# Optimization experiments

Hardware: AMD Instinct MI355X
Metric: run time of the kernel (lower is better)

Reference implementation:

```python
import jax, jax.numpy as jnp
import numpy as np

N_NODES = 100000
N_EDGES = 1600000
DIMS = [64, 64, 64, 32]  # [n_feat] + hid


def setup_inputs() -> dict:
    key = jax.random.key(0)
    ks = jax.random.split(key, 2 + 2 * (len(DIMS) - 1))
    x = jax.random.normal(ks[0], (N_NODES, DIMS[0]), dtype=jnp.float32)
    edge_index = jax.random.randint(ks[1], (2, N_EDGES), 0, N_NODES, dtype=jnp.int64)
    inp = {"x": x, "edge_index": edge_index}
    for i in range(len(DIMS) - 1):
        fan_in, fan_out = DIMS[i], DIMS[i + 1]
        scale = 1.0 / np.sqrt(fan_in)
        inp[f"W{i+1}"] = jax.random.normal(ks[2 + 2 * i], (fan_in, fan_out), dtype=jnp.float32) * scale
        inp[f"b{i+1}"] = jax.random.normal(ks[3 + 2 * i], (fan_out,), dtype=jnp.float32) * scale
    return inp


def _gcn_conv(x, W, b, src, dst, dis):
    # h = X W ; out[i] = sum_{j->i} norm_ij * h[j] + dis[i]^2 * h[i] + b
    h = x @ W
    norm = dis[src] * dis[dst]                      # [E]
    agg = jax.ops.segment_sum(h[src] * norm[:, None], dst, num_segments=x.shape[0])
    agg = agg + h * (dis * dis)[:, None]            # self-loop contribution
    return agg + b


def reference(x, edge_index, W1, b1, W2, b2, W3, b3):
    src, dst = edge_index[0], edge_index[1]
    n = x.shape[0]
    # degree with self-loops (edge weight 1), symmetric normalization
    deg = jax.ops.segment_sum(jnp.ones(src.shape[0], x.dtype), dst, num_segments=n) + 1.0
    dis = jax.lax.rsqrt(deg)
    h = jax.nn.relu(_gcn_conv(x, W1, b1, src, dst, dis))   # dropout is identity in eval
    h = jax.nn.relu(_gcn_conv(h, W2, b2, src, dst, dis))
    return _gcn_conv(h, W3, b3, src, dst, dis)
```

## Files before the change

### kernel.cpp

```cpp
#include <hip/hip_runtime.h>


typedef __attribute__((ext_vector_type(8))) _Float16 half8;
typedef __attribute__((ext_vector_type(4))) _Float16 half4;

static inline int cdiv(int a, int b) { return (a + b - 1) / b; }

#define ACHUNK 2048
#define BSHIFT 7
#define BMASK 127
#define MAXNBK 1024
#define SCAN_CHUNK 1024
#define BCAP 4096

__global__ __launch_bounds__(256)
void k_bucket_hist(const int* __restrict__ dst, int* __restrict__ counts_t,
                   int NBK, int NBA, int E) {
    __shared__ int cnt[MAXNBK];
    int t = threadIdx.x, b = blockIdx.x;
    for (int i = t; i < NBK; i += 256) cnt[i] = 0;
    __syncthreads();
    int e0 = b * ACHUNK;
#pragma unroll 8
    for (int j = 0; j < ACHUNK / 256; ++j) {
        int e = e0 + j * 256 + t;
        if (e < E) atomicAdd(&cnt[dst[e] >> BSHIFT], 1);
    }
    __syncthreads();
    for (int i = t; i < NBK; i += 256) counts_t[i * NBA + b] = cnt[i];
}

__global__ __launch_bounds__(256)
void k_scan_partial(const int* __restrict__ a, int* __restrict__ bsum, int n) {
    __shared__ int red[256];
    int t = threadIdx.x, b = blockIdx.x;
    int base = b * SCAN_CHUNK + t * 4;
    int s = 0;
#pragma unroll
    for (int j = 0; j < 4; ++j) { int i = base + j; if (i < n) s += a[i]; }
    red[t] = s;
    __syncthreads();
    for (int off = 128; off > 0; off >>= 1) {
        if (t < off) red[t] += red[t + off];
        __syncthreads();
    }
    if (t == 0) bsum[b] = red[0];
}

__global__ __launch_bounds__(256)
void k_scan_final(const int* __restrict__ a, const int* __restrict__ bsum,
                  int* __restrict__ out, int nb, int n) {
    __shared__ int sh[256];
    __shared__ int bb;
    int t = threadIdx.x, bk = blockIdx.x;
    int bv[4];
    int bt = 0;
#pragma unroll
    for (int j = 0; j < 4; ++j) {
        int i = 4 * t + j;
        bv[j] = (i < nb) ? bsum[i] : 0;
        bt += bv[j];
    }
    sh[t] = bt;
    __syncthreads();
    for (int off = 1; off < 256; off <<= 1) {
        int u = (t >= off) ? sh[t - off] : 0;
        __syncthreads();
        sh[t] += u;
        __syncthreads();
    }
    int bexcl = sh[t] - bt;
    if (bk == 0) {
        if (t == 0) bb = 0;
    } else {
        int q = bk - 1;
        if (t == (q >> 2)) {
            int s = bexcl;
#pragma unroll
            for (int j = 0; j < 4; ++j)
                if (j <= (q & 3)) s += bv[j];
            bb = s;
        }
    }
    __syncthreads();
    int bbase = bb;
    __syncthreads();
    int base = bk * SCAN_CHUNK + t * 4;
    int v[4];
    int s = 0;
#pragma unroll
    for (int j = 0; j < 4; ++j) {
        int i = base + j;
        v[j] = (i < n) ? a[i] : 0;
        s += v[j];
    }
    sh[t] = s;
    __syncthreads();
    for (int off = 1; off < 256; off <<= 1) {
        int u = (t >= off) ? sh[t - off] : 0;
        __syncthreads();
        sh[t] += u;
        __syncthreads();
    }
    int run = sh[t] - s + bbase;
#pragma unroll
    for (int j = 0; j < 4; ++j) {
        int i = base + j;
        if (i < n) { out[i] = run; run += v[j]; }
    }
}

__global__ __launch_bounds__(256)
void k_bucket_scatter(const int* __restrict__ src, const int* __restrict__ dst,
                      const int* __restrict__ offsets, unsigned* __restrict__ bucketed,
                      int NBK, int NBA, int E) {
    __shared__ int curs[MAXNBK];
    int t = threadIdx.x, b = blockIdx.x;
    for (int i = t; i < NBK; i += 256) curs[i] = offsets[i * NBA + b];
    __syncthreads();
    int e0 = b * ACHUNK;
#pragma unroll 8
    for (int j = 0; j < ACHUNK / 256; ++j) {
        int e = e0 + j * 256 + t;
        if (e < E) {
            int d = dst[e];
            int pos = atomicAdd(&curs[d >> BSHIFT], 1);
            bucketed[pos] = (unsigned)src[e] | ((unsigned)(d & BMASK) << 24);
        }
    }
}

__global__ __launch_bounds__(256)
void k_bucket_build(const unsigned* __restrict__ bucketed,
                    const int* __restrict__ offsets,
                    int* __restrict__ csr_src, int* __restrict__ row_start,
                    float* __restrict__ dis, int NBK, int NBA, int N, int E) {
    __shared__ int cnt[128];
    __shared__ int sc[128];
    __shared__ int srt[BCAP];
    int t = threadIdx.x, k = blockIdx.x;
    int base = offsets[k * NBA];
    int end = (k + 1 < NBK) ? offsets[(k + 1) * NBA] : E;
    if (t < 128) cnt[t] = 0;
    __syncthreads();
    for (int i = base + t; i < end; i += 256)
        atomicAdd(&cnt[bucketed[i] >> 24], 1);
    __syncthreads();
    int c = 0;
    if (t < 128) { c = cnt[t]; sc[t] = c; }
    __syncthreads();
    for (int off = 1; off < 128; off <<= 1) {
        int u = (t >= off && t < 128) ? sc[t - off] : 0;
        __syncthreads();
        if (t < 128) sc[t] += u;
        __syncthreads();
    }
    if (t < 128) {
        int excl = sc[t] - c;
        int node = (k << BSHIFT) + t;
        if (node < N) {
            row_start[node] = base + excl;
            dis[node] = rsqrtf(1.0f + (float)c);
        }
        cnt[t] = excl;
    }
    if (k == 0 && t == 0) row_start[N] = E;
    __syncthreads();
    int m = end - base;
    if (m <= BCAP) {
        for (int i = base + t; i < end; i += 256) {
            unsigned w = bucketed[i];
            int r = atomicAdd(&cnt[w >> 24], 1);
            srt[r] = (int)(w & 0xFFFFFFu);
        }
        __syncthreads();
        for (int idx = t; idx < m; idx += 256)
            csr_src[base + idx] = srt[idx];
    } else {
        for (int i = base + t; i < end; i += 256) {
            unsigned w = bucketed[i];
            int pos = base + atomicAdd(&cnt[w >> 24], 1);
            csr_src[pos] = (int)(w & 0xFFFFFFu);
        }
    }
}

template <int K, int M>
__global__ void k_gemm_f(const float* __restrict__ X, const float* __restrict__ W,
                         const float* __restrict__ dis, _Float16* __restrict__ H, int n) {
    constexpr int TPR = M / 8;
    constexpr int ROWS = 256 / TPR;
    constexpr int KP = K + 1;
    __shared__ float Ws[K * M];
    __shared__ float Xs[ROWS * KP];
    int tid = threadIdx.x;
    for (int idx = tid; idx < K * M / 4; idx += 256)
        ((float4*)Ws)[idx] = ((const float4*)W)[idx];
    int row0 = blockIdx.x * ROWS;
    for (int idx = tid; idx < ROWS * (K / 4); idx += 256) {
        int r = idx / (K / 4), kq = idx % (K / 4);
        int row = row0 + r;
        float4 vv = (row < n) ? ((const float4*)X)[(size_t)row * (K / 4) + kq]
                              : make_float4(0.f, 0.f, 0.f, 0.f);
        Xs[r * KP + kq * 4 + 0] = vv.x;
        Xs[r * KP + kq * 4 + 1] = vv.y;
        Xs[r * KP + kq * 4 + 2] = vv.z;
        Xs[r * KP + kq * 4 + 3] = vv.w;
    }
    __syncthreads();
    int r = tid / TPR, c0 = (tid % TPR) * 8;
    int row = row0 + r;
    if (row >= n) return;
    float4 a0 = make_float4(0.f, 0.f, 0.f, 0.f);
    float4 a1 = make_float4(0.f, 0.f, 0.f, 0.f);
#pragma unroll
    for (int k = 0; k < K; ++k) {
        float xv = Xs[r * KP + k];
        float4 w0 = ((const float4*)Ws)[(k * M + c0) / 4];
        float4 w1 = ((const float4*)Ws)[(k * M + c0) / 4 + 1];
        a0.x = fmaf(xv, w0.x, a0.x);
        a0.y = fmaf(xv, w0.y, a0.y);
        a0.z = fmaf(xv, w0.z, a0.z);
        a0.w = fmaf(xv, w0.w, a0.w);
        a1.x = fmaf(xv, w1.x, a1.x);
        a1.y = fmaf(xv, w1.y, a1.y);
        a1.z = fmaf(xv, w1.z, a1.z);
        a1.w = fmaf(xv, w1.w, a1.w);
    }
    float dn = dis[row];
    half8 hv;
    hv[0] = (_Float16)(a0.x * dn);
    hv[1] = (_Float16)(a0.y * dn);
    hv[2] = (_Float16)(a0.z * dn);
    hv[3] = (_Float16)(a0.w * dn);
    hv[4] = (_Float16)(a1.x * dn);
    hv[5] = (_Float16)(a1.y * dn);
    hv[6] = (_Float16)(a1.z * dn);
    hv[7] = (_Float16)(a1.w * dn);
    ((half8*)H)[(size_t)row * (M / 8) + c0 / 8] = hv;
}

template <int MOUT>
__global__ __launch_bounds__(256, 8)
void k_fused_agg_gemm(const _Float16* __restrict__ h, const float* __restrict__ dis,
                      const int* __restrict__ row_start, const int* __restrict__ csr_src,
                      const float* __restrict__ bagg, const float* __restrict__ W,
                      _Float16* __restrict__ H, int n) {
    constexpr int K = 64, KP = K + 1;
    __shared__ __align__(16) _Float16 Ws[K * MOUT];
    __shared__ float Xs[32 * KP];
    int tid = threadIdx.x;
    for (int idx = tid; idx < K * MOUT / 4; idx += 256) {
        float4 wv = ((const float4*)W)[idx];
        half4 h4;
        h4[0] = (_Float16)wv.x;
        h4[1] = (_Float16)wv.y;
        h4[2] = (_Float16)wv.z;
        h4[3] = (_Float16)wv.w;
        ((half4*)Ws)[idx] = h4;
    }

    int wave = tid >> 6, lane = tid & 63;
    int sub = lane >> 3, fl = lane & 7;
    int node0 = blockIdx.x * 32;
    int node = node0 + wave * 8 + sub;
    if (node < n) {
        const half8* h8 = (const half8*)h;
        float acc[8];
#pragma unroll
        for (int j = 0; j < 8; ++j) acc[j] = 0.f;
        int e = row_start[node], e1 = row_start[node + 1];
        for (; e + 7 < e1; e += 8) {
            int s0 = csr_src[e], s1 = csr_src[e + 1];
            int s2 = csr_src[e + 2], s3 = csr_src[e + 3];
            int s4 = csr_src[e + 4], s5 = csr_src[e + 5];
            int s6 = csr_src[e + 6], s7 = csr_src[e + 7];
            half8 v0 = h8[(size_t)s0 * 8 + fl];
            half8 v1 = h8[(size_t)s1 * 8 + fl];
            half8 v2 = h8[(size_t)s2 * 8 + fl];
            half8 v3 = h8[(size_t)s3 * 8 + fl];
            half8 v4 = h8[(size_t)s4 * 8 + fl];
            half8 v5 = h8[(size_t)s5 * 8 + fl];
            half8 v6 = h8[(size_t)s6 * 8 + fl];
            half8 v7 = h8[(size_t)s7 * 8 + fl];
#pragma unroll
            for (int j = 0; j < 8; ++j)
                acc[j] += (((float)v0[j] + (float)v1[j]) + ((float)v2[j] + (float)v3[j])) +
                          (((float)v4[j] + (float)v5[j]) + ((float)v6[j] + (float)v7[j]));
        }
        for (; e + 3 < e1; e += 4) {
            int s0 = csr_src[e], s1 = csr_src[e + 1];
            int s2 = csr_src[e + 2], s3 = csr_src[e + 3];
            half8 v0 = h8[(size_t)s0 * 8 + fl];
            half8 v1 = h8[(size_t)s1 * 8 + fl];
            half8 v2 = h8[(size_t)s2 * 8 + fl];
            half8 v3 = h8[(size_t)s3 * 8 + fl];
#pragma unroll
            for (int j = 0; j < 8; ++j)
                acc[j] += ((float)v0[j] + (float)v1[j]) + ((float)v2[j] + (float)v3[j]);
        }
        for (; e < e1; ++e) {
            int s0 = csr_src[e];
            half8 v0 = h8[(size_t)s0 * 8 + fl];
#pragma unroll
            for (int j = 0; j < 8; ++j) acc[j] += (float)v0[j];
        }
        float dn = dis[node];
        half8 hv = h8[(size_t)node * 8 + fl];
        float4 b0 = ((const float4*)bagg)[fl * 2];
        float4 b1 = ((const float4*)bagg)[fl * 2 + 1];
        int rrow = wave * 8 + sub;
        float* xp = &Xs[rrow * KP + fl * 8];
        xp[0] = fmaxf((acc[0] + (float)hv[0]) * dn + b0.x, 0.f);
        xp[1] = fmaxf((acc[1] + (float)hv[1]) * dn + b0.y, 0.f);
        xp[2] = fmaxf((acc[2] + (float)hv[2]) * dn + b0.z, 0.f);
        xp[3] = fmaxf((acc[3] + (float)hv[3]) * dn + b0.w, 0.f);
        xp[4] = fmaxf((acc[4] + (float)hv[4]) * dn + b1.x, 0.f);
        xp[5] = fmaxf((acc[5] + (float)hv[5]) * dn + b1.y, 0.f);
        xp[6] = fmaxf((acc[6] + (float)hv[6]) * dn + b1.z, 0.f);
        xp[7] = fmaxf((acc[7] + (float)hv[7]) * dn + b1.w, 0.f);
    }
    __syncthreads();

    constexpr int TPR = 8;
    constexpr int CPT = MOUT / TPR;
    int r = tid / TPR, c0 = (tid % TPR) * CPT;
    int row = node0 + r;
    if (row >= n) return;
    float4 a0 = make_float4(0.f, 0.f, 0.f, 0.f);
    float4 a1 = make_float4(0.f, 0.f, 0.f, 0.f);
#pragma unroll
    for (int k = 0; k < K; ++k) {
        float xv = Xs[r * KP + k];
        if constexpr (CPT == 8) {
            half8 w = ((const half8*)Ws)[(k * MOUT + c0) / 8];
            a0.x = fmaf(xv, (float)w[0], a0.x);
            a0.y = fmaf(xv, (float)w[1], a0.y);
            a0.z = fmaf(xv, (float)w[2], a0.z);
            a0.w = fmaf(xv, (float)w[3], a0.w);
            a1.x = fmaf(xv, (float)w[4], a1.x);
            a1.y = fmaf(xv, (float)w[5], a1.y);
            a1.z = fmaf(xv, (float)w[6], a1.z);
            a1.w = fmaf(xv, (float)w[7], a1.w);
        } else {
            half4 w = ((const half4*)Ws)[(k * MOUT + c0) / 4];
            a0.x = fmaf(xv, (float)w[0], a0.x);
            a0.y = fmaf(xv, (float)w[1], a0.y);
            a0.z = fmaf(xv, (float)w[2], a0.z);
            a0.w = fmaf(xv, (float)w[3], a0.w);
        }
    }
    float dn = dis[row];
    if constexpr (CPT == 8) {
        half8 hv;
        hv[0] = (_Float16)(a0.x * dn);
        hv[1] = (_Float16)(a0.y * dn);
        hv[2] = (_Float16)(a0.z * dn);
        hv[3] = (_Float16)(a0.w * dn);
        hv[4] = (_Float16)(a1.x * dn);
        hv[5] = (_Float16)(a1.y * dn);
        hv[6] = (_Float16)(a1.z * dn);
        hv[7] = (_Float16)(a1.w * dn);
        ((half8*)H)[(size_t)row * (MOUT / 8) + c0 / 8] = hv;
    } else {
        half4 hv;
        hv[0] = (_Float16)(a0.x * dn);
        hv[1] = (_Float16)(a0.y * dn);
        hv[2] = (_Float16)(a0.z * dn);
        hv[3] = (_Float16)(a0.w * dn);
        ((half4*)H)[(size_t)row * (MOUT / 4) + c0 / 4] = hv;
    }
}

__global__ __launch_bounds__(256, 8)
void k_aggregate32(const _Float16* __restrict__ h, const float* __restrict__ dis,
                   const int* __restrict__ row_start, const int* __restrict__ csr_src,
                   const float* __restrict__ b, float* __restrict__ out, int n) {
    constexpr int LPN = 4, NPW = 16;
    int gtid = blockIdx.x * blockDim.x + threadIdx.x;
    int wave = gtid >> 6;
    int lane = threadIdx.x & 63;
    int sub = lane / LPN, fl = lane % LPN;
    int node = wave * NPW + sub;
    if (node >= n) return;
    const half8* h8 = (const half8*)h;
    float acc[8];
#pragma unroll
    for (int j = 0; j < 8; ++j) acc[j] = 0.f;
    int e = row_start[node], e1 = row_start[node + 1];
    for (; e + 7 < e1; e += 8) {
        int s0 = csr_src[e], s1 = csr_src[e + 1];
        int s2 = csr_src[e + 2], s3 = csr_src[e + 3];
        int s4 = csr_src[e + 4], s5 = csr_src[e + 5];
        int s6 = csr_src[e + 6], s7 = csr_src[e + 7];
        half8 v0 = h8[(size_t)s0 * LPN + fl];
        half8 v1 = h8[(size_t)s1 * LPN + fl];
        half8 v2 = h8[(size_t)s2 * LPN + fl];
        half8 v3 = h8[(size_t)s3 * LPN + fl];
        half8 v4 = h8[(size_t)s4 * LPN + fl];
        half8 v5 = h8[(size_t)s5 * LPN + fl];
        half8 v6 = h8[(size_t)s6 * LPN + fl];
        half8 v7 = h8[(size_t)s7 * LPN + fl];
#pragma unroll
        for (int j = 0; j < 8; ++j)
            acc[j] += (((float)v0[j] + (float)v1[j]) + ((float)v2[j] + (float)v3[j])) +
                      (((float)v4[j] + (float)v5[j]) + ((float)v6[j] + (float)v7[j]));
    }
    for (; e + 3 < e1; e += 4) {
        int s0 = csr_src[e], s1 = csr_src[e + 1];
        int s2 = csr_src[e + 2], s3 = csr_src[e + 3];
        half8 v0 = h8[(size_t)s0 * LPN + fl];
        half8 v1 = h8[(size_t)s1 * LPN + fl];
        half8 v2 = h8[(size_t)s2 * LPN + fl];
        half8 v3 = h8[(size_t)s3 * LPN + fl];
#pragma unroll
        for (int j = 0; j < 8; ++j)
            acc[j] += ((float)v0[j] + (float)v1[j]) + ((float)v2[j] + (float)v3[j]);
    }
    for (; e < e1; ++e) {
        int s0 = csr_src[e];
        half8 v0 = h8[(size_t)s0 * LPN + fl];
#pragma unroll
        for (int j = 0; j < 8; ++j) acc[j] += (float)v0[j];
    }
    float dn = dis[node];
    half8 hv = h8[(size_t)node * LPN + fl];
    float4 b0 = ((const float4*)b)[fl * 2];
    float4 b1 = ((const float4*)b)[fl * 2 + 1];
    float4* op = (float4*)(out + ((size_t)node * LPN + fl) * 8);
    op[0] = make_float4((acc[0] + (float)hv[0]) * dn + b0.x,
                        (acc[1] + (float)hv[1]) * dn + b0.y,
                        (acc[2] + (float)hv[2]) * dn + b0.z,
                        (acc[3] + (float)hv[3]) * dn + b0.w);
    op[1] = make_float4((acc[4] + (float)hv[4]) * dn + b1.x,
                        (acc[5] + (float)hv[5]) * dn + b1.y,
                        (acc[6] + (float)hv[6]) * dn + b1.z,
                        (acc[7] + (float)hv[7]) * dn + b1.w);
}

extern "C" void kernel_launch(void* const* d_in, const int* in_sizes, int n_in,
                              void* d_out, int out_size, void* d_ws, size_t ws_size,
                              hipStream_t stream) {
    const float* x   = (const float*)d_in[0];
    const int*   ei  = (const int*)d_in[1];
    const float* W1  = (const float*)d_in[2];
    const float* b1  = (const float*)d_in[3];
    const float* W2  = (const float*)d_in[4];
    const float* b2  = (const float*)d_in[5];
    const float* W3  = (const float*)d_in[6];
    const float* b3  = (const float*)d_in[7];
    float* out = (float*)d_out;

    const int N = in_sizes[0] / 64;
    const int E = in_sizes[1] / 2;
    const int* src = ei;
    const int* dst = ei + E;

    const int NBK = cdiv(N, 128);
    const int NBA = cdiv(E, ACHUNK);
    const int nmat = NBK * NBA;
    const int nb = cdiv(nmat, SCAN_CHUNK);

    const size_t Np = (size_t)((N + 63) / 64) * 64;
    char* p = (char*)d_ws;
    int*      counts_t = (int*)p;      p += (size_t)nmat * sizeof(int);
    int*      offsets  = (int*)p;      p += (size_t)nmat * sizeof(int);
    int*      bsum     = (int*)p;      p += 1024 * sizeof(int);
    int*      row_start= (int*)p;      p += (Np + 64) * sizeof(int);
    float*    dis      = (float*)p;    p += Np * sizeof(float);
    unsigned* bucketed = (unsigned*)p; p += (size_t)E * sizeof(unsigned);
    int*      csr_src  = (int*)p;      p += (size_t)E * sizeof(int);
    _Float16* bufA     = (_Float16*)p; p += Np * 64 * sizeof(_Float16);
    _Float16* bufB     = (_Float16*)p; p += Np * 64 * sizeof(_Float16);
    (void)ws_size;

    const int B = 256;

    k_bucket_hist<<<NBA, B, 0, stream>>>(dst, counts_t, NBK, NBA, E);
    k_scan_partial<<<nb, B, 0, stream>>>(counts_t, bsum, nmat);
    k_scan_final<<<nb, B, 0, stream>>>(counts_t, bsum, offsets, nb, nmat);
    k_bucket_scatter<<<NBA, B, 0, stream>>>(src, dst, offsets, bucketed, NBK, NBA, E);
    k_bucket_build<<<NBK, B, 0, stream>>>(bucketed, offsets, csr_src, row_start, dis,
                                          NBK, NBA, N, E);

    k_gemm_f<64, 64><<<cdiv(N, 32), B, 0, stream>>>(x, W1, dis, bufA, N);
    k_fused_agg_gemm<64><<<cdiv(N, 32), B, 0, stream>>>(
        bufA, dis, row_start, csr_src, b1, W2, bufB, N);
    k_fused_agg_gemm<32><<<cdiv(N, 32), B, 0, stream>>>(
        bufB, dis, row_start, csr_src, b2, W3, bufA, N);
    k_aggregate32<<<cdiv(cdiv(N, 16) * 64, B), B, 0, stream>>>(
        bufA, dis, row_start, csr_src, b3, out, N);
}
```

Baseline: 296.7 us.

## Fuse CSR bucket build with first-layer GEMM and merge scan into one kernel

Widens each destination bucket to 256 nodes and enlarges edge chunks, which shrinks the count matrix. The two-pass scan becomes a single kernel in which every block recomputes the chunk totals with wave shuffles. The CSR bucket-build kernel now also runs the layer-1 X·W1 GEMM for its 256 nodes, reusing the per-node normalisation it just computed, which saves two kernel launches. The cost is that the fused kernel has only about 391 blocks, so the GEMM part loses parallelism, and larger buckets may overflow shared memory more often and fall back to the slower global-scatter path.

```diff
diff --git a/kernel.cpp b/kernel.cpp
--- a/kernel.cpp
+++ b/kernel.cpp
@@ -6,12 +6,10 @@
 
 static inline int cdiv(int a, int b) { return (a + b - 1) / b; }
 
-#define ACHUNK 2048
-#define BSHIFT 7
-#define BMASK 127
-#define MAXNBK 1024
+#define ACHUNK 8192
+#define MAXNBK 512
 #define SCAN_CHUNK 1024
-#define BCAP 4096
+#define BCAP 6144
 
 __global__ __launch_bounds__(256)
 void k_bucket_hist(const int* __restrict__ dst, int* __restrict__ counts_t,
@@ -24,44 +22,33 @@
 #pragma unroll 8
     for (int j = 0; j < ACHUNK / 256; ++j) {
         int e = e0 + j * 256 + t;
-        if (e < E) atomicAdd(&cnt[dst[e] >> BSHIFT], 1);
+        if (e < E) atomicAdd(&cnt[dst[e] >> 8], 1);
     }
     __syncthreads();
     for (int i = t; i < NBK; i += 256) counts_t[i * NBA + b] = cnt[i];
 }
 
 __global__ __launch_bounds__(256)
-void k_scan_partial(const int* __restrict__ a, int* __restrict__ bsum, int n) {
-    __shared__ int red[256];
-    int t = threadIdx.x, b = blockIdx.x;
-    int base = b * SCAN_CHUNK + t * 4;
-    int s = 0;
-#pragma unroll
-    for (int j = 0; j < 4; ++j) { int i = base + j; if (i < n) s += a[i]; }
-    red[t] = s;
-    __syncthreads();
-    for (int off = 128; off > 0; off >>= 1) {
-        if (t < off) red[t] += red[t + off];
-        __syncthreads();
-    }
-    if (t == 0) bsum[b] = red[0];
-}
-
-__global__ __launch_bounds__(256)
-void k_scan_final(const int* __restrict__ a, const int* __restrict__ bsum,
-                  int* __restrict__ out, int nb, int n) {
+void k_scan1(const int* __restrict__ a, int* __restrict__ out, int nb, int n) {
+    __shared__ int ct[256];
     __shared__ int sh[256];
-    __shared__ int bb;
     int t = threadIdx.x, bk = blockIdx.x;
-    int bv[4];
-    int bt = 0;
-#pragma unroll
-    for (int j = 0; j < 4; ++j) {
-        int i = 4 * t + j;
-        bv[j] = (i < nb) ? bsum[i] : 0;
-        bt += bv[j];
-    }
-    sh[t] = bt;
+    int wave = t >> 6, lane = t & 63;
+    for (int q = wave; q < nb; q += 4) {
+        int base = q * SCAN_CHUNK + lane * 16;
+        int s = 0;
+#pragma unroll
+        for (int j = 0; j < 16; ++j) {
+            int i = base + j;
+            if (i < n) s += a[i];
+        }
+#pragma unroll
+        for (int off = 32; off > 0; off >>= 1)
+            s += __shfl_xor(s, off, 64);
+        if (lane == 0) ct[q] = s;
+    }
+    __syncthreads();
+    sh[t] = (t < nb) ? ct[t] : 0;
     __syncthreads();
     for (int off = 1; off < 256; off <<= 1) {
         int u = (t >= off) ? sh[t - off] : 0;
@@ -69,21 +56,7 @@
         sh[t] += u;
         __syncthreads();
     }
-    int bexcl = sh[t] - bt;
-    if (bk == 0) {
-        if (t == 0) bb = 0;
-    } else {
-        int q = bk - 1;
-        if (t == (q >> 2)) {
-            int s = bexcl;
-#pragma unroll
-            for (int j = 0; j < 4; ++j)
-                if (j <= (q & 3)) s += bv[j];
-            bb = s;
-        }
-    }
-    __syncthreads();
-    int bbase = bb;
+    int bbase = (bk == 0) ? 0 : sh[bk - 1];
     __syncthreads();
     int base = bk * SCAN_CHUNK + t * 4;
     int v[4];
@@ -124,120 +97,128 @@
         int e = e0 + j * 256 + t;
         if (e < E) {
             int d = dst[e];
-            int pos = atomicAdd(&curs[d >> BSHIFT], 1);
-            bucketed[pos] = (unsigned)src[e] | ((unsigned)(d & BMASK) << 24);
+            int pos = atomicAdd(&curs[d >> 8], 1);
+            bucketed[pos] = (unsigned)src[e] | ((unsigned)(d & 255) << 24);
         }
     }
 }
 
 __global__ __launch_bounds__(256)
-void k_bucket_build(const unsigned* __restrict__ bucketed,
-                    const int* __restrict__ offsets,
-                    int* __restrict__ csr_src, int* __restrict__ row_start,
-                    float* __restrict__ dis, int NBK, int NBA, int N, int E) {
-    __shared__ int cnt[128];
-    __shared__ int sc[128];
-    __shared__ int srt[BCAP];
+void k_build_gemm(const unsigned* __restrict__ bucketed,
+                  const int* __restrict__ offsets,
+                  int* __restrict__ csr_src, int* __restrict__ row_start,
+                  float* __restrict__ dis, const float* __restrict__ X,
+                  const float* __restrict__ W1, _Float16* __restrict__ H,
+                  int NBK, int NBA, int N, int E) {
+    __shared__ __align__(16) char smem[26624];
+    __shared__ float disL[256];
     int t = threadIdx.x, k = blockIdx.x;
-    int base = offsets[k * NBA];
-    int end = (k + 1 < NBK) ? offsets[(k + 1) * NBA] : E;
-    if (t < 128) cnt[t] = 0;
-    __syncthreads();
-    for (int i = base + t; i < end; i += 256)
-        atomicAdd(&cnt[bucketed[i] >> 24], 1);
-    __syncthreads();
-    int c = 0;
-    if (t < 128) { c = cnt[t]; sc[t] = c; }
-    __syncthreads();
-    for (int off = 1; off < 128; off <<= 1) {
-        int u = (t >= off && t < 128) ? sc[t - off] : 0;
-        __syncthreads();
-        if (t < 128) sc[t] += u;
-        __syncthreads();
-    }
-    if (t < 128) {
+
+    {
+        int* cnt = (int*)smem;
+        int* sc  = cnt + 256;
+        int* srt = sc + 256;
+        int base = offsets[k * NBA];
+        int end = (k + 1 < NBK) ? offsets[(k + 1) * NBA] : E;
+        cnt[t] = 0;
+        __syncthreads();
+        for (int i = base + t; i < end; i += 256)
+            atomicAdd(&cnt[bucketed[i] >> 24], 1);
+        __syncthreads();
+        int c = cnt[t];
+        sc[t] = c;
+        __syncthreads();
+        for (int off = 1; off < 256; off <<= 1) {
+            int u = (t >= off) ? sc[t - off] : 0;
+            __syncthreads();
+            sc[t] += u;
+            __syncthreads();
+        }
         int excl = sc[t] - c;
-        int node = (k << BSHIFT) + t;
+        int node = k * 256 + t;
+        float dn = rsqrtf(1.0f + (float)c);
+        disL[t] = dn;
         if (node < N) {
             row_start[node] = base + excl;
-            dis[node] = rsqrtf(1.0f + (float)c);
-        }
+            dis[node] = dn;
+        }
+        if (k == 0 && t == 0) row_start[N] = E;
         cnt[t] = excl;
-    }
-    if (k == 0 && t == 0) row_start[N] = E;
-    __syncthreads();
-    int m = end - base;
-    if (m <= BCAP) {
-        for (int i = base + t; i < end; i += 256) {
-            unsigned w = bucketed[i];
-            int r = atomicAdd(&cnt[w >> 24], 1);
-            srt[r] = (int)(w & 0xFFFFFFu);
-        }
-        __syncthreads();
-        for (int idx = t; idx < m; idx += 256)
-            csr_src[base + idx] = srt[idx];
-    } else {
-        for (int i = base + t; i < end; i += 256) {
-            unsigned w = bucketed[i];
-            int pos = base + atomicAdd(&cnt[w >> 24], 1);
-            csr_src[pos] = (int)(w & 0xFFFFFFu);
-        }
-    }
-}
-
-template <int K, int M>
-__global__ void k_gemm_f(const float* __restrict__ X, const float* __restrict__ W,
-                         const float* __restrict__ dis, _Float16* __restrict__ H, int n) {
-    constexpr int TPR = M / 8;
-    constexpr int ROWS = 256 / TPR;
-    constexpr int KP = K + 1;
-    __shared__ float Ws[K * M];
-    __shared__ float Xs[ROWS * KP];
-    int tid = threadIdx.x;
-    for (int idx = tid; idx < K * M / 4; idx += 256)
-        ((float4*)Ws)[idx] = ((const float4*)W)[idx];
-    int row0 = blockIdx.x * ROWS;
-    for (int idx = tid; idx < ROWS * (K / 4); idx += 256) {
-        int r = idx / (K / 4), kq = idx % (K / 4);
-        int row = row0 + r;
-        float4 vv = (row < n) ? ((const float4*)X)[(size_t)row * (K / 4) + kq]
-                              : make_float4(0.f, 0.f, 0.f, 0.f);
-        Xs[r * KP + kq * 4 + 0] = vv.x;
-        Xs[r * KP + kq * 4 + 1] = vv.y;
-        Xs[r * KP + kq * 4 + 2] = vv.z;
-        Xs[r * KP + kq * 4 + 3] = vv.w;
-    }
-    __syncthreads();
-    int r = tid / TPR, c0 = (tid % TPR) * 8;
-    int row = row0 + r;
-    if (row >= n) return;
-    float4 a0 = make_float4(0.f, 0.f, 0.f, 0.f);
-    float4 a1 = make_float4(0.f, 0.f, 0.f, 0.f);
-#pragma unroll
-    for (int k = 0; k < K; ++k) {
-        float xv = Xs[r * KP + k];
-        float4 w0 = ((const float4*)Ws)[(k * M + c0) / 4];
-        float4 w1 = ((const float4*)Ws)[(k * M + c0) / 4 + 1];
-        a0.x = fmaf(xv, w0.x, a0.x);
-        a0.y = fmaf(xv, w0.y, a0.y);
-        a0.z = fmaf(xv, w0.z, a0.z);
-        a0.w = fmaf(xv, w0.w, a0.w);
-        a1.x = fmaf(xv, w1.x, a1.x);
-        a1.y = fmaf(xv, w1.y, a1.y);
-        a1.z = fmaf(xv, w1.z, a1.z);
-        a1.w = fmaf(xv, w1.w, a1.w);
-    }
-    float dn = dis[row];
-    half8 hv;
-    hv[0] = (_Float16)(a0.x * dn);
-    hv[1] = (_Float16)(a0.y * dn);
-    hv[2] = (_Float16)(a0.z * dn);
-    hv[3] = (_Float16)(a0.w * dn);
-    hv[4] = (_Float16)(a1.x * dn);
-    hv[5] = (_Float16)(a1.y * dn);
-    hv[6] = (_Float16)(a1.z * dn);
-    hv[7] = (_Float16)(a1.w * dn);
-    ((half8*)H)[(size_t)row * (M / 8) + c0 / 8] = hv;
+        __syncthreads();
+        int m = end - base;
+        if (m <= BCAP) {
+            for (int i = base + t; i < end; i += 256) {
+                unsigned w = bucketed[i];
+                int r = atomicAdd(&cnt[w >> 24], 1);
+                srt[r] = (int)(w & 0xFFFFFFu);
+            }
+            __syncthreads();
+            for (int idx = t; idx < m; idx += 256)
+                csr_src[base + idx] = srt[idx];
+        } else {
+            for (int i = base + t; i < end; i += 256) {
+                unsigned w = bucketed[i];
+                int pos = base + atomicAdd(&cnt[w >> 24], 1);
+                csr_src[pos] = (int)(w & 0xFFFFFFu);
+            }
+        }
+        __syncthreads();
+    }
+
+    {
+        float* Ws = (float*)smem;
+        float* Xs = Ws + 64 * 64;
+        constexpr int K = 64, KP = 65;
+        for (int idx = t; idx < K * 64 / 4; idx += 256)
+            ((float4*)Ws)[idx] = ((const float4*)W1)[idx];
+        int r = t / 8, c0 = (t % 8) * 8;
+        for (int rt = 0; rt < 8; ++rt) {
+            int row0 = k * 256 + rt * 32;
+            if (row0 >= N) break;
+            for (int idx = t; idx < 32 * (K / 4); idx += 256) {
+                int rr = idx / (K / 4), kq = idx % (K / 4);
+                int row = row0 + rr;
+                float4 vv = (row < N) ? ((const float4*)X)[(size_t)row * (K / 4) + kq]
+                                      : make_float4(0.f, 0.f, 0.f, 0.f);
+                Xs[rr * KP + kq * 4 + 0] = vv.x;
+                Xs[rr * KP + kq * 4 + 1] = vv.y;
+                Xs[rr * KP + kq * 4 + 2] = vv.z;
+                Xs[rr * KP + kq * 4 + 3] = vv.w;
+            }
+            __syncthreads();
+            int row = row0 + r;
+            if (row < N) {
+                float4 a0 = make_float4(0.f, 0.f, 0.f, 0.f);
+                float4 a1 = make_float4(0.f, 0.f, 0.f, 0.f);
+#pragma unroll
+                for (int kk = 0; kk < K; ++kk) {
+                    float xv = Xs[r * KP + kk];
+                    float4 w0 = ((const float4*)Ws)[(kk * 64 + c0) / 4];
+                    float4 w1 = ((const float4*)Ws)[(kk * 64 + c0) / 4 + 1];
+                    a0.x = fmaf(xv, w0.x, a0.x);
+                    a0.y = fmaf(xv, w0.y, a0.y);
+                    a0.z = fmaf(xv, w0.z, a0.z);
+                    a0.w = fmaf(xv, w0.w, a0.w);
+                    a1.x = fmaf(xv, w1.x, a1.x);
+                    a1.y = fmaf(xv, w1.y, a1.y);
+                    a1.z = fmaf(xv, w1.z, a1.z);
+                    a1.w = fmaf(xv, w1.w, a1.w);
+                }
+                float dn = disL[rt * 32 + r];
+                half8 hv;
+                hv[0] = (_Float16)(a0.x * dn);
+                hv[1] = (_Float16)(a0.y * dn);
+                hv[2] = (_Float16)(a0.z * dn);
+                hv[3] = (_Float16)(a0.w * dn);
+                hv[4] = (_Float16)(a1.x * dn);
+                hv[5] = (_Float16)(a1.y * dn);
+                hv[6] = (_Float16)(a1.z * dn);
+                hv[7] = (_Float16)(a1.w * dn);
+                ((half8*)H)[(size_t)row * 8 + c0 / 8] = hv;
+            }
+            __syncthreads();
+        }
+    }
 }
 
 template <int MOUT>
@@ -456,7 +437,7 @@
     const int* src = ei;
     const int* dst = ei + E;
 
-    const int NBK = cdiv(N, 128);
+    const int NBK = cdiv(N, 256);
     const int NBA = cdiv(E, ACHUNK);
     const int nmat = NBK * NBA;
     const int nb = cdiv(nmat, SCAN_CHUNK);
@@ -465,7 +446,6 @@
     char* p = (char*)d_ws;
     int*      counts_t = (int*)p;      p += (size_t)nmat * sizeof(int);
     int*      offsets  = (int*)p;      p += (size_t)nmat * sizeof(int);
-    int*      bsum     = (int*)p;      p += 1024 * sizeof(int);
     int*      row_start= (int*)p;      p += (Np + 64) * sizeof(int);
     float*    dis      = (float*)p;    p += Np * sizeof(float);
     unsigned* bucketed = (unsigned*)p; p += (size_t)E * sizeof(unsigned);
@@ -477,13 +457,11 @@
     const int B = 256;
 
     k_bucket_hist<<<NBA, B, 0, stream>>>(dst, counts_t, NBK, NBA, E);
-    k_scan_partial<<<nb, B, 0, stream>>>(counts_t, bsum, nmat);
-    k_scan_final<<<nb, B, 0, stream>>>(counts_t, bsum, offsets, nb, nmat);
+    k_scan1<<<nb, B, 0, stream>>>(counts_t, offsets, nb, nmat);
     k_bucket_scatter<<<NBA, B, 0, stream>>>(src, dst, offsets, bucketed, NBK, NBA, E);
-    k_bucket_build<<<NBK, B, 0, stream>>>(bucketed, offsets, csr_src, row_start, dis,
-                                          NBK, NBA, N, E);
-
-    k_gemm_f<64, 64><<<cdiv(N, 32), B, 0, stream>>>(x, W1, dis, bufA, N);
+    k_build_gemm<<<NBK, B, 0, stream>>>(bucketed, offsets, csr_src, row_start, dis,
+                                        x, W1, bufA, NBK, NBA, N, E);
+
     k_fused_agg_gemm<64><<<cdiv(N, 32), B, 0, stream>>>(
         bufA, dis, row_start, csr_src, b1, W2, bufB, N);
     k_fused_agg_gemm<32><<<cdiv(N, 32), B, 0, stream>>>(
```

Measured after the change: 339.3 us. 1.14x slower.
